# Performance work log

Hardware: AMD Instinct MI355X
Metric: run time of the kernel (lower is better)

## Reference

```python
import jax, jax.numpy as jnp
import numpy as np

# Fixed chemistry config (2 atom types):
#   type 0 (H): orbitals s,p        -> per-l counts [1,1],   block dim 1+3 = 4
#   type 1 (C): orbitals s,s,p,d    -> per-l counts [2,1,1], block dim 2+3+5 = 10
COMMON_AM = [0, 0, 1, 2]            # multiplicity-expanded union of angular momenta
ORBITAL_NUM = [[1, 1], [2, 1, 1]]
ORBITAL_SUM = [4, 10]
NUM_TYPES = 2
SQRT_LEN = len(COMMON_AM)


def _build_graph(rng, N, E_half):
    E_reg = 2 * E_half
    E = E_reg + N
    atom_type = rng.integers(0, NUM_TYPES, size=N).astype(np.int64)
    a = rng.integers(0, N, size=E_half)
    b = rng.integers(0, N, size=E_half)
    n1 = np.empty(E, dtype=np.int64); n2 = np.empty(E, dtype=np.int64)
    n1[0:E_reg:2] = a; n2[0:E_reg:2] = b          # edge 2i   : a->b
    n1[1:E_reg:2] = b; n2[1:E_reg:2] = a          # edge 2i+1 : b->a (its inverse)
    n1[E_reg:] = np.arange(N); n2[E_reg:] = np.arange(N)   # self edges (edge_include_sc)
    inv = np.empty(E, dtype=np.int64)
    inv[0:E_reg:2] = np.arange(1, E_reg, 2)
    inv[1:E_reg:2] = np.arange(0, E_reg, 2)
    inv[E_reg:] = np.arange(E_reg, E)
    S = rng.standard_normal((E, 3)).astype(np.float32)
    S[:, 0] += 2.0                                 # regular edges: nonzero shift
    S[E_reg:] = 0.0                                # self edges: zero shift
    sel = {}
    for t1 in range(NUM_TYPES):
        for t2 in range(NUM_TYPES):
            sel[(t1, t2)] = np.nonzero((atom_type[n1] == t1) & (atom_type[n2] == t2))[0].astype(np.int64)
    return atom_type, n1, n2, inv, S, sel


def setup_inputs() -> dict:
    rng = np.random.default_rng(0)
    N, E_half = 20000, 160000
    atom_type, n1, n2, inv, S, sel = _build_graph(rng, N, E_half)
    E = n1.shape[0]
    feat_dim = sum(2 * l + 1 for l in COMMON_AM) ** 2  # 100
    out = {
        'feature_node': jnp.asarray(rng.standard_normal((N, feat_dim)).astype(np.float32)),
        'feature_edge': jnp.asarray((0.1 * rng.standard_normal((E, feat_dim))).astype(np.float32)),
        'S_hop': jnp.asarray(S),
        'edge_index_hop': jnp.asarray(np.stack([n1, n2])),
        'AtomType': jnp.asarray(atom_type),
        'edge_inverse': jnp.asarray(inv),
    }
    for l1 in range(3):
        for l2 in range(3):
            # stand-in for cat_{l3=|l1-l2|..l1+l2} wigner_3j(l1,l2,l3): same shapes/math
            out[f'cg_{l1}_{l2}'] = jnp.asarray(
                (0.2 * rng.standard_normal(((2 * l1 + 1), (2 * l2 + 1), (2 * l1 + 1) * (2 * l2 + 1)))).astype(np.float32))
    for (t1, t2), idx in sel.items():
        out[f'edge_sel_{t1}{t2}'] = jnp.asarray(idx)
    return out


def _forward(feature_node, feature_edge, S_hop, cg, n1, n2, edge_inverse, sel):
    E = feature_edge.shape[0]
    # self-connection injection (edge_include_sc=True): each node has exactly one
    # self edge (n1==n2 and |S_hop|<1e-6); node features are added on those rows.
    is_self = (n1 == n2) & (jnp.linalg.norm(S_hop, axis=-1) < 1e-6)
    feature_edge = feature_edge + jnp.where(is_self[:, None], feature_node[n1], 0.0)

    # DirectSum -> DirectProduct: per-(l1,l2) contraction with CG tensors
    blocks, offset = [], 0
    for l1 in COMMON_AM:
        for l2 in COMMON_AM:
            size = (2 * l1 + 1) * (2 * l2 + 1)
            blocks.append(jnp.einsum('nk,ijk->nij', feature_edge[:, offset:offset + size], cg[(l1, l2)]))
            offset += size

    # find_Hblock: gather blocks per atom-type pair into dense sub-Hamiltonians
    hams = []
    g2b = jnp.zeros(E, dtype=jnp.int32)
    for t1 in range(NUM_TYPES):
        for t2 in range(NUM_TYPES):
            s = sel[(t1, t2)]
            ham = jnp.zeros((s.shape[0], ORBITAL_SUM[t1], ORBITAL_SUM[t2]), feature_edge.dtype)
            nl1 = list(ORBITAL_NUM[t1])
            boff, roff = 0, 0
            for l1 in COMMON_AM:
                if len(nl1) < l1 + 1 or nl1[l1] == 0:
                    boff += SQRT_LEN
                    continue
                nl1[l1] -= 1
                coff = 0
                nl2 = list(ORBITAL_NUM[t2])
                for l2 in COMMON_AM:
                    if len(nl2) < l2 + 1 or nl2[l2] == 0:
                        boff += 1
                        continue
                    nl2[l2] -= 1
                    ham = ham.at[:, roff:roff + 2 * l1 + 1, coff:coff + 2 * l2 + 1].set(blocks[boff][s])
                    boff += 1
                    coff += 2 * l2 + 1
                roff += 2 * l1 + 1
            hams.append(ham)
            g2b = g2b.at[s].set(jnp.arange(s.shape[0], dtype=jnp.int32))

    # hermitian symmetrization across (t1,t2)/(t2,t1) block lists
    for t1 in range(NUM_TYPES):
        for t2 in range(t1, NUM_TYPES):
            i12, i21 = t1 * NUM_TYPES + t2, t2 * NUM_TYPES + t1
            eb21 = g2b[edge_inverse[sel[(t1, t2)]]]
            hams[i12] = 0.5 * (hams[i12] + jnp.swapaxes(hams[i21][eb21], -2, -1))
            if t1 != t2:
                eb12 = g2b[edge_inverse[sel[(t2, t1)]]]
                hams[i21] = jnp.swapaxes(hams[i12][eb12], -2, -1)
    return hams, g2b


def reference(feature_node, feature_edge, S_hop, edge_index_hop, AtomType, edge_inverse,
              cg_0_0, cg_0_1, cg_0_2, cg_1_0, cg_1_1, cg_1_2, cg_2_0, cg_2_1, cg_2_2,
              edge_sel_00, edge_sel_01, edge_sel_10, edge_sel_11):
    cg = {(0, 0): cg_0_0, (0, 1): cg_0_1, (0, 2): cg_0_2,
          (1, 0): cg_1_0, (1, 1): cg_1_1, (1, 2): cg_1_2,
          (2, 0): cg_2_0, (2, 1): cg_2_1, (2, 2): cg_2_2}
    sel = {(0, 0): edge_sel_00, (0, 1): edge_sel_01, (1, 0): edge_sel_10, (1, 1): edge_sel_11}
    n1, n2 = edge_index_hop[0], edge_index_hop[1]
    hams, g2b = _forward(feature_node, feature_edge, S_hop, cg, n1, n2, edge_inverse, sel)
    return (*hams, g2b)
```

## Files before the change

kernel.cpp:

```cpp
#include <hip/hip_runtime.h>

struct CgPtrs { const float* p[9]; };
struct Desc  { int s00, s01, s10, s11, Ereg, E; };

__host__ __device__ constexpr int DSL(int s){ return s<2?1:(s==2?3:5); }
__host__ __device__ constexpr int PRE(int s){ return s==0?0:(s==1?1:(s==2?2:5)); }
__host__ __device__ constexpr int LSL(int s){ return s<2?0:(s==2?1:2); }
__host__ __device__ constexpr int OFT(int a,int b){ return PRE(a)*10 + DSL(a)*PRE(b); }

__global__ __launch_bounds__(256) void prep_kernel(
    const int* __restrict__ sel00, const int* __restrict__ sel01,
    const int* __restrict__ sel10, const int* __restrict__ sel11,
    Desc d, int* __restrict__ rank, float* __restrict__ og)
{
    int u = blockIdx.x*256 + threadIdx.x;
    if (u < d.s00){ int e=sel00[u]; rank[e]=(u<<2)|0; og[e]=(float)u; return; } u-=d.s00;
    if (u < d.s01){ int e=sel01[u]; rank[e]=(u<<2)|1; og[e]=(float)u; return; } u-=d.s01;
    if (u < d.s10){ int e=sel10[u]; rank[e]=(u<<2)|2; og[e]=(float)u; return; } u-=d.s10;
    if (u < d.s11){ int e=sel11[u]; rank[e]=(u<<2)|3; og[e]=(float)u; return; }
}

template<int S1,int S2,int I0,int NR>
__device__ __forceinline__ void rows_chunk(const float* __restrict__ x,
    const float* __restrict__ y, const CgPtrs& cg, float* acc)
{
    constexpr int d1=DSL(S1), d2=DSL(S2), K=d1*d2;
    constexpr int xo=OFT(S1,S2), yo=OFT(S2,S1), c0=PRE(S2);
    const float* __restrict__ wA = cg.p[LSL(S1)*3+LSL(S2)];
    const float* __restrict__ wB = cg.p[LSL(S2)*3+LSL(S1)];
    float xc[K], yc[K];
    #pragma unroll
    for (int k=0;k<K;++k) xc[k]=x[xo+k];
    #pragma unroll
    for (int k=0;k<K;++k) yc[k]=y[yo+k];
    #pragma unroll
    for (int r=0;r<NR;++r){
        #pragma unroll
        for (int j=0;j<d2;++j){
            float a = acc[r*10 + c0 + j];
            #pragma unroll
            for (int k=0;k<K;++k) a = fmaf(xc[k], wA[((I0+r)*d2+j)*K+k], a);
            #pragma unroll
            for (int k=0;k<K;++k) a = fmaf(yc[k], wB[(j*d1+I0+r)*K+k], a);
            acc[r*10 + c0 + j] = a;
        }
    }
}

template<int S1,int I0,int NR>
__device__ __forceinline__ void band_all(const float* x, const float* y,
                                         const CgPtrs& cg, float* acc)
{
    rows_chunk<S1,0,I0,NR>(x,y,cg,acc);
    rows_chunk<S1,1,I0,NR>(x,y,cg,acc);
    rows_chunk<S1,2,I0,NR>(x,y,cg,acc);
    rows_chunk<S1,3,I0,NR>(x,y,cg,acc);
}

__device__ __forceinline__ void stcols(float* p, const float* ar){
    *(float4*)p = make_float4(ar[0], ar[2], ar[3], ar[4]);
}
__device__ __forceinline__ void strow10(float* p, const float* ar){
    #pragma unroll
    for (int j=0;j<5;++j) *(float2*)(p+2*j) = make_float2(ar[2*j], ar[2*j+1]);
}

__global__ __launch_bounds__(256,6) void ham_kernel(
    const float* __restrict__ fn, const float* __restrict__ fe,
    const int* __restrict__ rank,
    CgPtrs cg, Desc d, float* __restrict__ out)
{
    __shared__ float xs[64*101];
    float* o00 = out;
    float* o01 = o00 + (size_t)d.s00*16;
    float* o10 = o01 + (size_t)d.s01*40;
    float* o11 = o10 + (size_t)d.s10*40;

    const int e0  = blockIdx.x*64;
    const int tid = threadIdx.x;
    const int nE  = min(64, d.E - e0);

    for (int idx = tid; idx < nE*25; idx += 256){
        const int row = idx/25, q = idx - 25*row;
        const int e = e0 + row;
        float4 v = *(const float4*)(fe + (size_t)e*100 + 4*q);
        if (e >= d.Ereg){
            float4 w = *(const float4*)(fn + (size_t)(e - d.Ereg)*100 + 4*q);
            v.x += w.x; v.y += w.y; v.z += w.z; v.w += w.w;
        }
        float* dst = xs + row*101 + 4*q;
        dst[0]=0.5f*v.x; dst[1]=0.5f*v.y; dst[2]=0.5f*v.z; dst[3]=0.5f*v.w;
    }
    __syncthreads();

    const int lane = tid & 63;
    const int grp  = ((tid>>6) + blockIdx.x) & 3;
    const int e = e0 + lane;
    const bool act = (lane < nE);
    float acc[40];
    #pragma unroll
    for (int i=0;i<40;++i) acc[i]=0.f;

    int rk=0, c=0;
    if (act){
        const int pk = rank[e];
        rk = pk >> 2; c = pk & 3;
        const float* x = xs + lane*101;
        const float* y = (e >= d.Ereg) ? x : xs + (lane^1)*101;
        if      (grp==0){ band_all<0,0,1>(x,y,cg,acc);
                          band_all<1,0,1>(x,y,cg,acc+10);
                          band_all<2,0,2>(x,y,cg,acc+20); }
        else if (grp==1){ band_all<2,2,1>(x,y,cg,acc);
                          band_all<3,4,1>(x,y,cg,acc+10); }
        else if (grp==2){ band_all<3,0,2>(x,y,cg,acc); }
        else            { band_all<3,2,2>(x,y,cg,acc); }
    }

    if (act){
        if (grp==0){
            if (c==3){ float* o=o11+(size_t)rk*100;
                #pragma unroll
                for (int u=0;u<10;++u)
                    *(float4*)(o+4*u) = make_float4(acc[4*u],acc[4*u+1],acc[4*u+2],acc[4*u+3]); }
            else if (c==2){ float* o=o10+(size_t)rk*40;
                stcols(o+0,acc); stcols(o+4,acc+10); stcols(o+8,acc+20); stcols(o+12,acc+30); }
            else if (c==1){ float* o=o01+(size_t)rk*40;
                strow10(o+0,acc); strow10(o+10,acc+20); strow10(o+20,acc+30); }
            else { float* o=o00+(size_t)rk*16;
                stcols(o+0,acc); stcols(o+4,acc+20); stcols(o+8,acc+30); }
        } else if (grp==1){
            if (c==3){ float* o=o11+(size_t)rk*100;
                strow10(o+40,acc); strow10(o+90,acc+10); }
            else if (c==2){ float* o=o10+(size_t)rk*40;
                stcols(o+16,acc); stcols(o+36,acc+10); }
            else if (c==1){ float* o=o01+(size_t)rk*40;
                strow10(o+30,acc); }
            else { float* o=o00+(size_t)rk*16; stcols(o+12,acc); }
        } else if (grp==2){
            if (c==3){ float* o=o11+(size_t)rk*100;
                strow10(o+50,acc); strow10(o+60,acc+10); }
            else if (c==2){ float* o=o10+(size_t)rk*40;
                stcols(o+20,acc); stcols(o+24,acc+10); }
        } else {
            if (c==3){ float* o=o11+(size_t)rk*100;
                strow10(o+70,acc); strow10(o+80,acc+10); }
            else if (c==2){ float* o=o10+(size_t)rk*40;
                stcols(o+28,acc); stcols(o+32,acc+10); }
        }
    }
}

extern "C" void kernel_launch(void* const* d_in, const int* in_sizes, int n_in,
                              void* d_out, int out_size, void* d_ws, size_t ws_size,
                              hipStream_t stream)
{
    const float* fn  = (const float*)d_in[0];
    const float* fe  = (const float*)d_in[1];
    CgPtrs cg;
    for (int i = 0; i < 9; ++i) cg.p[i] = (const float*)d_in[6 + i];
    const int* sel00 = (const int*)d_in[15];
    const int* sel01 = (const int*)d_in[16];
    const int* sel10 = (const int*)d_in[17];
    const int* sel11 = (const int*)d_in[18];

    const int N = in_sizes[0] / 100;
    const int E = in_sizes[3] / 2;

    Desc d;
    d.s00 = in_sizes[15]; d.s01 = in_sizes[16]; d.s10 = in_sizes[17]; d.s11 = in_sizes[18];
    d.Ereg = E - N;
    d.E = E;

    float* out = (float*)d_out;
    float* og  = out + (size_t)d.s00*16 + (size_t)d.s01*40 + (size_t)d.s10*40 + (size_t)d.s11*100;
    int* rank = (int*)d_ws;

    prep_kernel<<<(E + 255)/256, 256, 0, stream>>>(sel00, sel01, sel10, sel11, d, rank, og);
    ham_kernel <<<(E + 63)/64,   256, 0, stream>>>(fn, fe, rank, cg, d, out);
}
```

Before: 113.2 us.

## Split work across eight wavefronts and exchange transpose terms via lane shuffles

Doubles the block to 512 threads and splits each edge's Hamiltonian block into eight row groups, one per wavefront, so each wavefront holds at most 15 accumulators instead of 40. The symmetrization term from the inverse edge is now computed locally as a transposed contraction and swapped with the neighbouring lane through __shfl_xor, instead of reading the paired edge's features from shared memory. The aim is to cut register pressure, raise occupancy and balance work across wavefronts. The cost is a larger block, more partial stores, and inactive tail lanes that must still join the shuffle, which is why the early return comes after it.

```diff
diff --git a/kernel.cpp b/kernel.cpp
--- a/kernel.cpp
+++ b/kernel.cpp
@@ -20,52 +20,148 @@
     if (u < d.s11){ int e=sel11[u]; rank[e]=(u<<2)|3; og[e]=(float)u; return; }
 }
 
-template<int S1,int S2,int I0,int NR>
-__device__ __forceinline__ void rows_chunk(const float* __restrict__ x,
-    const float* __restrict__ y, const CgPtrs& cg, float* acc)
-{
-    constexpr int d1=DSL(S1), d2=DSL(S2), K=d1*d2;
-    constexpr int xo=OFT(S1,S2), yo=OFT(S2,S1), c0=PRE(S2);
-    const float* __restrict__ wA = cg.p[LSL(S1)*3+LSL(S2)];
-    const float* __restrict__ wB = cg.p[LSL(S2)*3+LSL(S1)];
-    float xc[K], yc[K];
+template<int S1,int S2,int I0,int AB>
+__device__ __forceinline__ void pA(const float* __restrict__ x, const CgPtrs& cg, float* acc){
+    constexpr int d1=DSL(S1), d2=DSL(S2), K=d1*d2, xo=OFT(S1,S2);
+    const float* __restrict__ w = cg.p[LSL(S1)*3+LSL(S2)];
+    float xc[K];
     #pragma unroll
     for (int k=0;k<K;++k) xc[k]=x[xo+k];
     #pragma unroll
-    for (int k=0;k<K;++k) yc[k]=y[yo+k];
-    #pragma unroll
-    for (int r=0;r<NR;++r){
+    for (int j=0;j<d2;++j){
+        float a=acc[AB+j];
         #pragma unroll
-        for (int j=0;j<d2;++j){
-            float a = acc[r*10 + c0 + j];
-            #pragma unroll
-            for (int k=0;k<K;++k) a = fmaf(xc[k], wA[((I0+r)*d2+j)*K+k], a);
-            #pragma unroll
-            for (int k=0;k<K;++k) a = fmaf(yc[k], wB[(j*d1+I0+r)*K+k], a);
-            acc[r*10 + c0 + j] = a;
-        }
-    }
-}
-
-template<int S1,int I0,int NR>
-__device__ __forceinline__ void band_all(const float* x, const float* y,
-                                         const CgPtrs& cg, float* acc)
-{
-    rows_chunk<S1,0,I0,NR>(x,y,cg,acc);
-    rows_chunk<S1,1,I0,NR>(x,y,cg,acc);
-    rows_chunk<S1,2,I0,NR>(x,y,cg,acc);
-    rows_chunk<S1,3,I0,NR>(x,y,cg,acc);
-}
-
-__device__ __forceinline__ void stcols(float* p, const float* ar){
-    *(float4*)p = make_float4(ar[0], ar[2], ar[3], ar[4]);
-}
-__device__ __forceinline__ void strow10(float* p, const float* ar){
-    #pragma unroll
-    for (int j=0;j<5;++j) *(float2*)(p+2*j) = make_float2(ar[2*j], ar[2*j+1]);
-}
-
-__global__ __launch_bounds__(256,6) void ham_kernel(
+        for (int k=0;k<K;++k) a=fmaf(xc[k], w[(I0*d2+j)*K+k], a);
+        acc[AB+j]=a;
+    }
+}
+template<int S1,int S2,int I0,int AB>
+__device__ __forceinline__ void pT(const float* __restrict__ x, const CgPtrs& cg, float* acc){
+    constexpr int d1=DSL(S1), d2=DSL(S2), K=d1*d2, xo=OFT(S2,S1);
+    const float* __restrict__ w = cg.p[LSL(S2)*3+LSL(S1)];
+    float xc[K];
+    #pragma unroll
+    for (int k=0;k<K;++k) xc[k]=x[xo+k];
+    #pragma unroll
+    for (int j=0;j<d2;++j){
+        float a=acc[AB+j];
+        #pragma unroll
+        for (int k=0;k<K;++k) a=fmaf(xc[k], w[(j*d1+I0)*K+k], a);
+        acc[AB+j]=a;
+    }
+}
+
+template<int S1,int I0,int AB>
+__device__ __forceinline__ void rowfullA(const float* x, const CgPtrs& cg, float* a){
+    pA<S1,0,I0,AB+0>(x,cg,a); pA<S1,1,I0,AB+1>(x,cg,a);
+    pA<S1,2,I0,AB+2>(x,cg,a); pA<S1,3,I0,AB+5>(x,cg,a);
+}
+template<int S1,int I0,int AB>
+__device__ __forceinline__ void rowfullT(const float* x, const CgPtrs& cg, float* a){
+    pT<S1,0,I0,AB+0>(x,cg,a); pT<S1,1,I0,AB+1>(x,cg,a);
+    pT<S1,2,I0,AB+2>(x,cg,a); pT<S1,3,I0,AB+5>(x,cg,a);
+}
+template<int S1,int I0,int AB>
+__device__ __forceinline__ void rowrestA(const float* x, const CgPtrs& cg, float* a){
+    pA<S1,0,I0,AB+0>(x,cg,a); pA<S1,1,I0,AB+1>(x,cg,a); pA<S1,2,I0,AB+2>(x,cg,a);
+}
+template<int S1,int I0,int AB>
+__device__ __forceinline__ void rowrestT(const float* x, const CgPtrs& cg, float* a){
+    pT<S1,0,I0,AB+0>(x,cg,a); pT<S1,1,I0,AB+1>(x,cg,a); pT<S1,2,I0,AB+2>(x,cg,a);
+}
+
+__device__ __forceinline__ void st5o(float* p, const float* a){
+    p[0]=a[0]; *(float2*)(p+1)=make_float2(a[1],a[2]); *(float2*)(p+3)=make_float2(a[3],a[4]);
+}
+__device__ __forceinline__ void st5e(float* p, const float* a){
+    *(float2*)(p)=make_float2(a[0],a[1]); *(float2*)(p+2)=make_float2(a[2],a[3]); p[4]=a[4];
+}
+__device__ __forceinline__ void st10f(float* p, const float* a){
+    #pragma unroll
+    for (int j=0;j<5;++j) *(float2*)(p+2*j)=make_float2(a[2*j],a[2*j+1]);
+}
+__device__ __forceinline__ void st4p(float* p, const float* a){
+    *(float4*)p = make_float4(a[0],a[2],a[3],a[4]);
+}
+
+template<int G>
+__device__ __forceinline__ void do_group(
+    const float* x, bool slf, bool act, int rk, int c, const CgPtrs& cg,
+    float* __restrict__ o00, float* __restrict__ o01,
+    float* __restrict__ o10, float* __restrict__ o11)
+{
+    float c1[15], tt[15];
+    #pragma unroll
+    for (int u=0;u<15;++u){ c1[u]=0.f; tt[u]=0.f; }
+
+    if constexpr (G==0){ pA<3,3,0,0>(x,cg,c1); rowfullA<0,0,5>(x,cg,c1);
+                         pT<3,3,0,0>(x,cg,tt); rowfullT<0,0,5>(x,cg,tt); }
+    if constexpr (G==1){ pA<3,3,1,0>(x,cg,c1); rowfullA<1,0,5>(x,cg,c1);
+                         pT<3,3,1,0>(x,cg,tt); rowfullT<1,0,5>(x,cg,tt); }
+    if constexpr (G==2){ pA<3,3,2,0>(x,cg,c1); rowrestA<3,3,5>(x,cg,c1);
+                         pT<3,3,2,0>(x,cg,tt); rowrestT<3,3,5>(x,cg,tt); }
+    if constexpr (G==3){ pA<3,3,3,0>(x,cg,c1); rowrestA<3,4,5>(x,cg,c1);
+                         pT<3,3,3,0>(x,cg,tt); rowrestT<3,4,5>(x,cg,tt); }
+    if constexpr (G==4){ pA<3,3,4,0>(x,cg,c1);
+                         pT<3,3,4,0>(x,cg,tt); }
+    if constexpr (G==5){ rowfullA<2,0,0>(x,cg,c1); rowrestA<3,0,10>(x,cg,c1);
+                         rowfullT<2,0,0>(x,cg,tt); rowrestT<3,0,10>(x,cg,tt); }
+    if constexpr (G==6){ rowfullA<2,1,0>(x,cg,c1); rowrestA<3,1,10>(x,cg,c1);
+                         rowfullT<2,1,0>(x,cg,tt); rowrestT<3,1,10>(x,cg,tt); }
+    if constexpr (G==7){ rowfullA<2,2,0>(x,cg,c1); rowrestA<3,2,10>(x,cg,c1);
+                         rowfullT<2,2,0>(x,cg,tt); rowrestT<3,2,10>(x,cg,tt); }
+
+    constexpr int NA = (G==2||G==3)?10:((G==4)?5:15);
+    float acc[15];
+    #pragma unroll
+    for (int u=0;u<NA;++u){
+        float tv = __shfl_xor(tt[u],1);
+        acc[u] = c1[u] + (slf ? tt[u] : tv);
+    }
+    if (!act) return;
+
+    if constexpr (G==0){
+        if (c==3){ float* o=o11+(size_t)rk*100; st5o(o+55,acc); st10f(o+0,acc+5); }
+        else if (c==2){ st4p(o10+(size_t)rk*40+0,  acc+5); }
+        else if (c==1){ st10f(o01+(size_t)rk*40+0, acc+5); }
+        else          { st4p(o00+(size_t)rk*16+0,  acc+5); }
+    }
+    if constexpr (G==1){
+        if (c==3){ float* o=o11+(size_t)rk*100; st5o(o+65,acc); st10f(o+10,acc+5); }
+        else if (c==2){ st4p(o10+(size_t)rk*40+4, acc+5); }
+    }
+    if constexpr (G==2){
+        if (c==3){ float* o=o11+(size_t)rk*100; st5o(o+75,acc); st5e(o+80,acc+5); }
+        else if (c==2){ st4p(o10+(size_t)rk*40+32, acc+5); }
+    }
+    if constexpr (G==3){
+        if (c==3){ float* o=o11+(size_t)rk*100; st5o(o+85,acc); st5e(o+90,acc+5); }
+        else if (c==2){ st4p(o10+(size_t)rk*40+36, acc+5); }
+    }
+    if constexpr (G==4){
+        if (c==3){ st5o(o11+(size_t)rk*100+95, acc); }
+    }
+    if constexpr (G==5){
+        if (c==3){ float* o=o11+(size_t)rk*100; st10f(o+20,acc); st5e(o+50,acc+10); }
+        else if (c==2){ st4p(o10+(size_t)rk*40+8, acc); st4p(o10+(size_t)rk*40+20, acc+10); }
+        else if (c==1){ st10f(o01+(size_t)rk*40+10, acc); }
+        else          { st4p(o00+(size_t)rk*16+4, acc); }
+    }
+    if constexpr (G==6){
+        if (c==3){ float* o=o11+(size_t)rk*100; st10f(o+30,acc); st5e(o+60,acc+10); }
+        else if (c==2){ st4p(o10+(size_t)rk*40+12, acc); st4p(o10+(size_t)rk*40+24, acc+10); }
+        else if (c==1){ st10f(o01+(size_t)rk*40+20, acc); }
+        else          { st4p(o00+(size_t)rk*16+8, acc); }
+    }
+    if constexpr (G==7){
+        if (c==3){ float* o=o11+(size_t)rk*100; st10f(o+40,acc); st5e(o+70,acc+10); }
+        else if (c==2){ st4p(o10+(size_t)rk*40+16, acc); st4p(o10+(size_t)rk*40+28, acc+10); }
+        else if (c==1){ st10f(o01+(size_t)rk*40+30, acc); }
+        else          { st4p(o00+(size_t)rk*16+12, acc); }
+    }
+}
+
+__global__ __launch_bounds__(512,6) void ham_kernel(
     const float* __restrict__ fn, const float* __restrict__ fe,
     const int* __restrict__ rank,
     CgPtrs cg, Desc d, float* __restrict__ out)
@@ -80,7 +176,7 @@
     const int tid = threadIdx.x;
     const int nE  = min(64, d.E - e0);
 
-    for (int idx = tid; idx < nE*25; idx += 256){
+    for (int idx = tid; idx < nE*25; idx += 512){
         const int row = idx/25, q = idx - 25*row;
         const int e = e0 + row;
         float4 v = *(const float4*)(fe + (size_t)e*100 + 4*q);
@@ -94,60 +190,23 @@
     __syncthreads();
 
     const int lane = tid & 63;
-    const int grp  = ((tid>>6) + blockIdx.x) & 3;
+    const int grp  = tid >> 6;
     const int e = e0 + lane;
     const bool act = (lane < nE);
-    float acc[40];
-    #pragma unroll
-    for (int i=0;i<40;++i) acc[i]=0.f;
-
-    int rk=0, c=0;
-    if (act){
-        const int pk = rank[e];
-        rk = pk >> 2; c = pk & 3;
-        const float* x = xs + lane*101;
-        const float* y = (e >= d.Ereg) ? x : xs + (lane^1)*101;
-        if      (grp==0){ band_all<0,0,1>(x,y,cg,acc);
-                          band_all<1,0,1>(x,y,cg,acc+10);
-                          band_all<2,0,2>(x,y,cg,acc+20); }
-        else if (grp==1){ band_all<2,2,1>(x,y,cg,acc);
-                          band_all<3,4,1>(x,y,cg,acc+10); }
-        else if (grp==2){ band_all<3,0,2>(x,y,cg,acc); }
-        else            { band_all<3,2,2>(x,y,cg,acc); }
-    }
-
-    if (act){
-        if (grp==0){
-            if (c==3){ float* o=o11+(size_t)rk*100;
-                #pragma unroll
-                for (int u=0;u<10;++u)
-                    *(float4*)(o+4*u) = make_float4(acc[4*u],acc[4*u+1],acc[4*u+2],acc[4*u+3]); }
-            else if (c==2){ float* o=o10+(size_t)rk*40;
-                stcols(o+0,acc); stcols(o+4,acc+10); stcols(o+8,acc+20); stcols(o+12,acc+30); }
-            else if (c==1){ float* o=o01+(size_t)rk*40;
-                strow10(o+0,acc); strow10(o+10,acc+20); strow10(o+20,acc+30); }
-            else { float* o=o00+(size_t)rk*16;
-                stcols(o+0,acc); stcols(o+4,acc+20); stcols(o+8,acc+30); }
-        } else if (grp==1){
-            if (c==3){ float* o=o11+(size_t)rk*100;
-                strow10(o+40,acc); strow10(o+90,acc+10); }
-            else if (c==2){ float* o=o10+(size_t)rk*40;
-                stcols(o+16,acc); stcols(o+36,acc+10); }
-            else if (c==1){ float* o=o01+(size_t)rk*40;
-                strow10(o+30,acc); }
-            else { float* o=o00+(size_t)rk*16; stcols(o+12,acc); }
-        } else if (grp==2){
-            if (c==3){ float* o=o11+(size_t)rk*100;
-                strow10(o+50,acc); strow10(o+60,acc+10); }
-            else if (c==2){ float* o=o10+(size_t)rk*40;
-                stcols(o+20,acc); stcols(o+24,acc+10); }
-        } else {
-            if (c==3){ float* o=o11+(size_t)rk*100;
-                strow10(o+70,acc); strow10(o+80,acc+10); }
-            else if (c==2){ float* o=o10+(size_t)rk*40;
-                stcols(o+28,acc); stcols(o+32,acc+10); }
-        }
-    }
+    const bool slf = (e >= d.Ereg);
+    const int pk = act ? rank[e] : 0;
+    const int rk = pk >> 2;
+    const int c  = pk & 3;
+    const float* x = xs + lane*101;
+
+    if      (grp==0) do_group<0>(x,slf,act,rk,c,cg,o00,o01,o10,o11);
+    else if (grp==1) do_group<1>(x,slf,act,rk,c,cg,o00,o01,o10,o11);
+    else if (grp==2) do_group<2>(x,slf,act,rk,c,cg,o00,o01,o10,o11);
+    else if (grp==3) do_group<3>(x,slf,act,rk,c,cg,o00,o01,o10,o11);
+    else if (grp==4) do_group<4>(x,slf,act,rk,c,cg,o00,o01,o10,o11);
+    else if (grp==5) do_group<5>(x,slf,act,rk,c,cg,o00,o01,o10,o11);
+    else if (grp==6) do_group<6>(x,slf,act,rk,c,cg,o00,o01,o10,o11);
+    else             do_group<7>(x,slf,act,rk,c,cg,o00,o01,o10,o11);
 }
 
 extern "C" void kernel_launch(void* const* d_in, const int* in_sizes, int n_in,
@@ -176,5 +235,5 @@
     int* rank = (int*)d_ws;
 
     prep_kernel<<<(E + 255)/256, 256, 0, stream>>>(sel00, sel01, sel10, sel11, d, rank, og);
-    ham_kernel <<<(E + 63)/64,   256, 0, stream>>>(fn, fe, rank, cg, d, out);
-}
+    ham_kernel <<<(E + 63)/64,   512, 0, stream>>>(fn, fe, rank, cg, d, out);
+}
```

Result: slower. 360.9 us (+218.7%).
